# Performance work log

Measured on AMD Instinct MI355X. Metric: run time of the kernel, lower is better.

## Reference

```python
import jax, jax.numpy as jnp
import numpy as np

B = 512        # batch size
N = 4096       # number of scores per row (init arg n)
K = 256        # top-k (init arg k)
EPS = 0.1      # sinkhorn entropic regularization
MAX_ITER = 200 # sinkhorn iterations
PAD = 1e-16


def setup_inputs() -> dict:
    key = jax.random.key(0)
    scores = jax.random.normal(key, (B, N), dtype=jnp.float32)
    return {"scores": scores}


def reference(scores):
    b = scores.shape[0]
    dt = scores.dtype
    anchors = jnp.array([0.0, 1.0], dtype=dt).reshape(1, 2, 1)
    mu = jnp.full((1, N), 1.0 / N, dtype=dt)
    nu = jnp.array([K / N, (N - K) / N], dtype=dt).reshape(1, 2)

    s = scores.reshape(b, 1, N)              # [b,1,n]
    C = (s - anchors) ** 2                   # [b,2,n]
    C = C / C.max()                          # global max over whole tensor (as in torch)
    G = jnp.exp(-C / EPS)                    # [b,2,n]

    u0 = jnp.ones((b, 2), dtype=dt)
    v0 = jnp.ones((b, N), dtype=dt)

    def body(carry, _):
        u, v = carry
        u = nu / (jnp.einsum('bkn,bn->bk', G, v) + PAD)   # [b,2]
        v = mu / (jnp.einsum('bkn,bk->bn', G, u) + PAD)   # [b,n]
        return (u, v), None

    (u, v), _ = jax.lax.scan(body, (u0, v0), None, length=MAX_ITER)
    P = u[:, :, None] * G * v[:, None, :]    # [b,2,n] transport plan
    return P
```

## Files before the change

kernel.cpp:

```cpp
#include <hip/hip_runtime.h>


#define NROWS 512
#define NCOLS 4096
#define KSEL 256
#define EPSREG 0.1f
#define NEWTON_ITERS 12

__device__ __forceinline__ float fastrcp(float x) {
#if __has_builtin(__builtin_amdgcn_rcpf)
    return __builtin_amdgcn_rcpf(x);
#else
    return 1.0f / x;
#endif
}

__global__ __launch_bounds__(256) void kmax_kernel(const float4* __restrict__ s4,
                                                   float* __restrict__ blkmax) {
    const int tid = blockIdx.x * 256 + threadIdx.x;
    float m = 0.f;
#pragma unroll
    for (int j = 0; j < 8; ++j) {
        float4 v = s4[tid + 65536 * j];
        m = fmaxf(m, fmaxf(v.x * v.x, (v.x - 1.f) * (v.x - 1.f)));
        m = fmaxf(m, fmaxf(v.y * v.y, (v.y - 1.f) * (v.y - 1.f)));
        m = fmaxf(m, fmaxf(v.z * v.z, (v.z - 1.f) * (v.z - 1.f)));
        m = fmaxf(m, fmaxf(v.w * v.w, (v.w - 1.f) * (v.w - 1.f)));
    }
#pragma unroll
    for (int off = 32; off >= 1; off >>= 1)
        m = fmaxf(m, __shfl_xor(m, off, 64));
    __shared__ float wmax[4];
    if ((threadIdx.x & 63) == 0) wmax[threadIdx.x >> 6] = m;
    __syncthreads();
    if (threadIdx.x == 0)
        blkmax[blockIdx.x] = fmaxf(fmaxf(wmax[0], wmax[1]), fmaxf(wmax[2], wmax[3]));
}

__global__ __launch_bounds__(256) void sinkhorn_kernel(const float* __restrict__ s,
                                                       const float* __restrict__ blkmax,
                                                       float* __restrict__ out) {
    const int b   = blockIdx.x;
    const int tid = threadIdx.x;
    const int wv  = tid >> 6;
    const int ln  = tid & 63;

    __shared__ float ldsm[4];
    __shared__ float lds[2][8];

    float m = blkmax[tid];
#pragma unroll
    for (int off = 32; off >= 1; off >>= 1)
        m = fmaxf(m, __shfl_xor(m, off, 64));
    if (ln == 0) ldsm[wv] = m;

    const float4* srow = (const float4*)(s + (size_t)b * NCOLS);
    float4 v[4];
#pragma unroll
    for (int j = 0; j < 4; ++j) v[j] = srow[tid + 256 * j];

    __syncthreads();
    const float M     = fmaxf(fmaxf(ldsm[0], ldsm[1]), fmaxf(ldsm[2], ldsm[3]));
    const float alpha = 1.0f / (M * EPSREG);
    const float c2    = -2.0f * alpha;

    float t[16];
    float sumt = 0.f;
#pragma unroll
    for (int j = 0; j < 4; ++j) {
        float xs[4] = {v[j].x, v[j].y, v[j].z, v[j].w};
#pragma unroll
        for (int e = 0; e < 4; ++e) {
            float tt = __expf(fmaf(xs[e], c2, alpha));
            t[4 * j + e] = tt;
            sumt += tt;
        }
    }

#pragma unroll
    for (int off = 32; off >= 1; off >>= 1)
        sumt += __shfl_xor(sumt, off, 64);
    if (ln == 0) lds[1][wv * 2] = sumt;
    __syncthreads();
    sumt = lds[1][0] + lds[1][2] + lds[1][4] + lds[1][6];

    float rho = (float)KSEL / sumt;

#pragma unroll 1
    for (int it = 0; it < NEWTON_ITERS; ++it) {
        float a = 0.f, q = 0.f;
#pragma unroll
        for (int e = 0; e < 16; ++e) {
            float w = fastrcp(fmaf(rho, t[e], 1.0f));
            a += w;
            q = fmaf(w, w, q);
        }
#pragma unroll
        for (int off = 32; off >= 1; off >>= 1) {
            a += __shfl_xor(a, off, 64);
            q += __shfl_xor(q, off, 64);
        }
        const int ph = it & 1;
        if (ln == 0) { lds[ph][wv * 2] = a; lds[ph][wv * 2 + 1] = q; }
        __syncthreads();
        a = lds[ph][0] + lds[ph][2] + lds[ph][4] + lds[ph][6];
        q = lds[ph][1] + lds[ph][3] + lds[ph][5] + lds[ph][7];
        rho += ((float)(KSEL - NCOLS) + a) * rho / (a - q);
    }

    const float MU = 1.0f / (float)NCOLS;
    float4* o0 = (float4*)(out + (size_t)b * 2 * NCOLS);
    float4* o1 = (float4*)(out + (size_t)b * 2 * NCOLS + NCOLS);
#pragma unroll
    for (int j = 0; j < 4; ++j) {
        float r0[4], r1[4];
#pragma unroll
        for (int e = 0; e < 4; ++e) {
            float w  = fastrcp(fmaf(rho, t[4 * j + e], 1.0f));
            float p1 = MU * w;
            r1[e] = p1;
            r0[e] = MU - p1;
        }
        o0[tid + 256 * j] = make_float4(r0[0], r0[1], r0[2], r0[3]);
        o1[tid + 256 * j] = make_float4(r1[0], r1[1], r1[2], r1[3]);
    }
}

extern "C" void kernel_launch(void* const* d_in, const int* in_sizes, int n_in,
                              void* d_out, int out_size, void* d_ws, size_t ws_size,
                              hipStream_t stream) {
    const float* scores = (const float*)d_in[0];
    float* out = (float*)d_out;
    float* blkmax = (float*)d_ws;

    hipLaunchKernelGGL(kmax_kernel, dim3(256), dim3(256), 0, stream,
                       (const float4*)scores, blkmax);
    hipLaunchKernelGGL(sinkhorn_kernel, dim3(NROWS), dim3(256), 0, stream,
                       scores, blkmax, out);
}
```

Measured before the change: 76.03 us.

## Fuse global max into sinkhorn kernel via cooperative grid sync

Merges the separate max-reduction kernel into the main kernel. Each block computes its own row max from the scores it already loaded, writes it to workspace, does a grid-wide sync, then reduces all 512 row maxima. This removes a second kernel launch and a second read of the whole score tensor. It also cuts the Newton iterations from 12 to 8, which lowers per-row compute but risks accuracy if the iteration has not converged. The cooperative launch requires all 512 blocks to be resident at once.

```diff
diff --git a/kernel.cpp b/kernel.cpp
--- a/kernel.cpp
+++ b/kernel.cpp
@@ -1,11 +1,14 @@
 #include <hip/hip_runtime.h>
+#include <hip/hip_cooperative_groups.h>
+
+namespace cg = cooperative_groups;
 
 
 #define NROWS 512
 #define NCOLS 4096
 #define KSEL 256
 #define EPSREG 0.1f
-#define NEWTON_ITERS 12
+#define NEWTON_ITERS 8
 
 __device__ __forceinline__ float fastrcp(float x) {
 #if __has_builtin(__builtin_amdgcn_rcpf)
@@ -15,50 +18,48 @@
 #endif
 }
 
-__global__ __launch_bounds__(256) void kmax_kernel(const float4* __restrict__ s4,
-                                                   float* __restrict__ blkmax) {
-    const int tid = blockIdx.x * 256 + threadIdx.x;
-    float m = 0.f;
-#pragma unroll
-    for (int j = 0; j < 8; ++j) {
-        float4 v = s4[tid + 65536 * j];
-        m = fmaxf(m, fmaxf(v.x * v.x, (v.x - 1.f) * (v.x - 1.f)));
-        m = fmaxf(m, fmaxf(v.y * v.y, (v.y - 1.f) * (v.y - 1.f)));
-        m = fmaxf(m, fmaxf(v.z * v.z, (v.z - 1.f) * (v.z - 1.f)));
-        m = fmaxf(m, fmaxf(v.w * v.w, (v.w - 1.f) * (v.w - 1.f)));
-    }
-#pragma unroll
-    for (int off = 32; off >= 1; off >>= 1)
-        m = fmaxf(m, __shfl_xor(m, off, 64));
-    __shared__ float wmax[4];
-    if ((threadIdx.x & 63) == 0) wmax[threadIdx.x >> 6] = m;
-    __syncthreads();
-    if (threadIdx.x == 0)
-        blkmax[blockIdx.x] = fmaxf(fmaxf(wmax[0], wmax[1]), fmaxf(wmax[2], wmax[3]));
-}
-
-__global__ __launch_bounds__(256) void sinkhorn_kernel(const float* __restrict__ s,
-                                                       const float* __restrict__ blkmax,
-                                                       float* __restrict__ out) {
+__global__ __launch_bounds__(256) void sinkhorn_fused(const float* __restrict__ s,
+                                                      float* __restrict__ rowmax,
+                                                      float* __restrict__ out) {
     const int b   = blockIdx.x;
     const int tid = threadIdx.x;
     const int wv  = tid >> 6;
     const int ln  = tid & 63;
 
     __shared__ float ldsm[4];
+    __shared__ float ldss[4];
     __shared__ float lds[2][8];
-
-    float m = blkmax[tid];
-#pragma unroll
-    for (int off = 32; off >= 1; off >>= 1)
-        m = fmaxf(m, __shfl_xor(m, off, 64));
-    if (ln == 0) ldsm[wv] = m;
 
     const float4* srow = (const float4*)(s + (size_t)b * NCOLS);
     float4 v[4];
 #pragma unroll
     for (int j = 0; j < 4; ++j) v[j] = srow[tid + 256 * j];
 
+    float m = 0.f;
+#pragma unroll
+    for (int j = 0; j < 4; ++j) {
+        float xs[4] = {v[j].x, v[j].y, v[j].z, v[j].w};
+#pragma unroll
+        for (int e = 0; e < 4; ++e) {
+            float x = xs[e];
+            m = fmaxf(m, fmaxf(x * x, (x - 1.f) * (x - 1.f)));
+        }
+    }
+#pragma unroll
+    for (int off = 32; off >= 1; off >>= 1)
+        m = fmaxf(m, __shfl_xor(m, off, 64));
+    if (ln == 0) ldsm[wv] = m;
+    __syncthreads();
+    if (tid == 0)
+        rowmax[b] = fmaxf(fmaxf(ldsm[0], ldsm[1]), fmaxf(ldsm[2], ldsm[3]));
+
+    cg::this_grid().sync();
+
+    m = fmaxf(rowmax[tid], rowmax[tid + 256]);
+#pragma unroll
+    for (int off = 32; off >= 1; off >>= 1)
+        m = fmaxf(m, __shfl_xor(m, off, 64));
+    if (ln == 0) ldsm[wv] = m;
     __syncthreads();
     const float M     = fmaxf(fmaxf(ldsm[0], ldsm[1]), fmaxf(ldsm[2], ldsm[3]));
     const float alpha = 1.0f / (M * EPSREG);
@@ -76,13 +77,12 @@
             sumt += tt;
         }
     }
-
 #pragma unroll
     for (int off = 32; off >= 1; off >>= 1)
         sumt += __shfl_xor(sumt, off, 64);
-    if (ln == 0) lds[1][wv * 2] = sumt;
+    if (ln == 0) ldss[wv] = sumt;
     __syncthreads();
-    sumt = lds[1][0] + lds[1][2] + lds[1][4] + lds[1][6];
+    sumt = ldss[0] + ldss[1] + ldss[2] + ldss[3];
 
     float rho = (float)KSEL / sumt;
 
@@ -131,10 +131,9 @@
                               hipStream_t stream) {
     const float* scores = (const float*)d_in[0];
     float* out = (float*)d_out;
-    float* blkmax = (float*)d_ws;
+    float* rowmax = (float*)d_ws;
 
-    hipLaunchKernelGGL(kmax_kernel, dim3(256), dim3(256), 0, stream,
-                       (const float4*)scores, blkmax);
-    hipLaunchKernelGGL(sinkhorn_kernel, dim3(NROWS), dim3(256), 0, stream,
-                       scores, blkmax, out);
+    void* args[] = {(void*)&scores, (void*)&rowmax, (void*)&out};
+    hipLaunchCooperativeKernel((const void*)sinkhorn_fused, dim3(NROWS), dim3(256),
+                               args, 0, stream);
 }
```

New measurement: 112.5 us. +48.0%, slower.

## Widen sinkhorn blocks to 1024 threads, spread max pass, halve Newton iterations

Applied to the files above, without the earlier changes.

The per-row solver kernel now uses 1024 threads, each owning one float4 instead of four, which shortens per-thread work and register use. The global-max pre-pass runs on 1024 blocks with two loads per thread instead of 256 blocks with eight. The Newton iteration count for the dual variable drops from 12 to 6, which removes half the block-wide reduction and barrier rounds but relies on Newton converging within 6 steps, a possible accuracy risk. Cross-wave reductions now read LDS partials through float4 loads.

```diff
diff --git a/kernel.cpp b/kernel.cpp
--- a/kernel.cpp
+++ b/kernel.cpp
@@ -5,7 +5,8 @@
 #define NCOLS 4096
 #define KSEL 256
 #define EPSREG 0.1f
-#define NEWTON_ITERS 12
+#define NEWTON_ITERS 6
+#define KMAX_BLOCKS 1024
 
 __device__ __forceinline__ float fastrcp(float x) {
 #if __has_builtin(__builtin_amdgcn_rcpf)
@@ -20,8 +21,8 @@
     const int tid = blockIdx.x * 256 + threadIdx.x;
     float m = 0.f;
 #pragma unroll
-    for (int j = 0; j < 8; ++j) {
-        float4 v = s4[tid + 65536 * j];
+    for (int j = 0; j < 2; ++j) {
+        float4 v = s4[tid + 262144 * j];
         m = fmaxf(m, fmaxf(v.x * v.x, (v.x - 1.f) * (v.x - 1.f)));
         m = fmaxf(m, fmaxf(v.y * v.y, (v.y - 1.f) * (v.y - 1.f)));
         m = fmaxf(m, fmaxf(v.z * v.z, (v.z - 1.f) * (v.z - 1.f)));
@@ -37,52 +38,58 @@
         blkmax[blockIdx.x] = fmaxf(fmaxf(wmax[0], wmax[1]), fmaxf(wmax[2], wmax[3]));
 }
 
-__global__ __launch_bounds__(256) void sinkhorn_kernel(const float* __restrict__ s,
-                                                       const float* __restrict__ blkmax,
-                                                       float* __restrict__ out) {
+__global__ __launch_bounds__(1024) void sinkhorn_kernel(const float* __restrict__ s,
+                                                        const float* __restrict__ blkmax,
+                                                        float* __restrict__ out) {
     const int b   = blockIdx.x;
     const int tid = threadIdx.x;
     const int wv  = tid >> 6;
     const int ln  = tid & 63;
 
-    __shared__ float ldsm[4];
-    __shared__ float lds[2][8];
+    __shared__ __align__(16) float ldsm[16];
+    __shared__ __align__(16) float ldss[16];
+    __shared__ __align__(16) float lds[2][32];
+
+    const float4* srow = (const float4*)(s + (size_t)b * NCOLS);
+    const float4 v = srow[tid];
 
     float m = blkmax[tid];
 #pragma unroll
     for (int off = 32; off >= 1; off >>= 1)
         m = fmaxf(m, __shfl_xor(m, off, 64));
     if (ln == 0) ldsm[wv] = m;
-
-    const float4* srow = (const float4*)(s + (size_t)b * NCOLS);
-    float4 v[4];
-#pragma unroll
-    for (int j = 0; j < 4; ++j) v[j] = srow[tid + 256 * j];
-
     __syncthreads();
-    const float M     = fmaxf(fmaxf(ldsm[0], ldsm[1]), fmaxf(ldsm[2], ldsm[3]));
-    const float alpha = 1.0f / (M * EPSREG);
+    {
+        const float4* p = (const float4*)ldsm;
+        float4 a0 = p[0], a1 = p[1], a2 = p[2], a3 = p[3];
+        m = fmaxf(fmaxf(fmaxf(a0.x, a0.y), fmaxf(a0.z, a0.w)),
+                  fmaxf(fmaxf(a1.x, a1.y), fmaxf(a1.z, a1.w)));
+        m = fmaxf(m, fmaxf(fmaxf(fmaxf(a2.x, a2.y), fmaxf(a2.z, a2.w)),
+                           fmaxf(fmaxf(a3.x, a3.y), fmaxf(a3.z, a3.w))));
+    }
+    const float alpha = 1.0f / (m * EPSREG);
     const float c2    = -2.0f * alpha;
 
-    float t[16];
+    float t[4];
+    const float xs[4] = {v.x, v.y, v.z, v.w};
     float sumt = 0.f;
 #pragma unroll
-    for (int j = 0; j < 4; ++j) {
-        float xs[4] = {v[j].x, v[j].y, v[j].z, v[j].w};
-#pragma unroll
-        for (int e = 0; e < 4; ++e) {
-            float tt = __expf(fmaf(xs[e], c2, alpha));
-            t[4 * j + e] = tt;
-            sumt += tt;
-        }
+    for (int e = 0; e < 4; ++e) {
+        float tt = __expf(fmaf(xs[e], c2, alpha));
+        t[e] = tt;
+        sumt += tt;
     }
-
 #pragma unroll
     for (int off = 32; off >= 1; off >>= 1)
         sumt += __shfl_xor(sumt, off, 64);
-    if (ln == 0) lds[1][wv * 2] = sumt;
+    if (ln == 0) ldss[wv] = sumt;
     __syncthreads();
-    sumt = lds[1][0] + lds[1][2] + lds[1][4] + lds[1][6];
+    {
+        const float4* p = (const float4*)ldss;
+        float4 a0 = p[0], a1 = p[1], a2 = p[2], a3 = p[3];
+        sumt = (a0.x + a0.y + a0.z + a0.w) + (a1.x + a1.y + a1.z + a1.w)
+             + (a2.x + a2.y + a2.z + a2.w) + (a3.x + a3.y + a3.z + a3.w);
+    }
 
     float rho = (float)KSEL / sumt;
 
@@ -90,7 +97,7 @@
     for (int it = 0; it < NEWTON_ITERS; ++it) {
         float a = 0.f, q = 0.f;
 #pragma unroll
-        for (int e = 0; e < 16; ++e) {
+        for (int e = 0; e < 4; ++e) {
             float w = fastrcp(fmaf(rho, t[e], 1.0f));
             a += w;
             q = fmaf(w, w, q);
@@ -103,27 +110,30 @@
         const int ph = it & 1;
         if (ln == 0) { lds[ph][wv * 2] = a; lds[ph][wv * 2 + 1] = q; }
         __syncthreads();
-        a = lds[ph][0] + lds[ph][2] + lds[ph][4] + lds[ph][6];
-        q = lds[ph][1] + lds[ph][3] + lds[ph][5] + lds[ph][7];
+        a = 0.f; q = 0.f;
+        const float4* p = (const float4*)lds[ph];
+#pragma unroll
+        for (int r = 0; r < 8; ++r) {
+            float4 f = p[r];
+            a += f.x + f.z;
+            q += f.y + f.w;
+        }
         rho += ((float)(KSEL - NCOLS) + a) * rho / (a - q);
     }
 
     const float MU = 1.0f / (float)NCOLS;
     float4* o0 = (float4*)(out + (size_t)b * 2 * NCOLS);
     float4* o1 = (float4*)(out + (size_t)b * 2 * NCOLS + NCOLS);
+    float r0[4], r1[4];
 #pragma unroll
-    for (int j = 0; j < 4; ++j) {
-        float r0[4], r1[4];
-#pragma unroll
-        for (int e = 0; e < 4; ++e) {
-            float w  = fastrcp(fmaf(rho, t[4 * j + e], 1.0f));
-            float p1 = MU * w;
-            r1[e] = p1;
-            r0[e] = MU - p1;
-        }
-        o0[tid + 256 * j] = make_float4(r0[0], r0[1], r0[2], r0[3]);
-        o1[tid + 256 * j] = make_float4(r1[0], r1[1], r1[2], r1[3]);
+    for (int e = 0; e < 4; ++e) {
+        float w  = fastrcp(fmaf(rho, t[e], 1.0f));
+        float p1 = MU * w;
+        r1[e] = p1;
+        r0[e] = MU - p1;
     }
+    o0[tid] = make_float4(r0[0], r0[1], r0[2], r0[3]);
+    o1[tid] = make_float4(r1[0], r1[1], r1[2], r1[3]);
 }
 
 extern "C" void kernel_launch(void* const* d_in, const int* in_sizes, int n_in,
@@ -133,8 +143,8 @@
     float* out = (float*)d_out;
     float* blkmax = (float*)d_ws;
 
-    hipLaunchKernelGGL(kmax_kernel, dim3(256), dim3(256), 0, stream,
+    hipLaunchKernelGGL(kmax_kernel, dim3(KMAX_BLOCKS), dim3(256), 0, stream,
                        (const float4*)scores, blkmax);
-    hipLaunchKernelGGL(sinkhorn_kernel, dim3(NROWS), dim3(256), 0, stream,
+    hipLaunchKernelGGL(sinkhorn_kernel, dim3(NROWS), dim3(1024), 0, stream,
                        scores, blkmax, out);
 }
```

Result: slower. 78.69 us (+3.5%).
